# Optimization experiments

Measured on AMD Instinct MI355X. Metric: run time of the kernel, lower is better.

The kernel has to match this reference:

```python
import jax, jax.numpy as jnp
import numpy as np

NEMB = 512
NEMBDIM = 64
NHIDDEN = 1024
NINPUT = 784
COMMIT_COST = 0.25


def setup_inputs() -> dict:
    key = jax.random.key(0)
    ks = jax.random.split(key, 16)
    B = 32768
    x = jax.random.uniform(ks[0], (B, NINPUT), dtype=jnp.float32)
    # codebook: uniform(-1/nemb, 1/nemb) as in torch init
    emb = jax.random.uniform(ks[1], (NEMB, NEMBDIM), dtype=jnp.float32,
                             minval=-1.0 / NEMB, maxval=1.0 / NEMB)
    s = 0.02
    We1 = jax.random.normal(ks[2], (NHIDDEN, NINPUT), dtype=jnp.float32) * s
    be1 = jnp.zeros((NHIDDEN,), jnp.float32)
    We2 = jax.random.normal(ks[3], (NHIDDEN, NHIDDEN), dtype=jnp.float32) * s
    be2 = jnp.zeros((NHIDDEN,), jnp.float32)
    We3 = jax.random.normal(ks[4], (NEMBDIM, NHIDDEN), dtype=jnp.float32) * s
    be3 = jnp.zeros((NEMBDIM,), jnp.float32)
    Wd1 = jax.random.normal(ks[5], (NHIDDEN, NEMBDIM), dtype=jnp.float32) * s
    bd1 = jnp.zeros((NHIDDEN,), jnp.float32)
    Wd2 = jax.random.normal(ks[6], (NHIDDEN, NHIDDEN), dtype=jnp.float32) * s
    bd2 = jnp.zeros((NHIDDEN,), jnp.float32)
    Wd3 = jax.random.normal(ks[7], (NINPUT, NHIDDEN), dtype=jnp.float32) * s
    bd3 = jnp.zeros((NINPUT,), jnp.float32)
    return dict(x=x, emb=emb, We1=We1, be1=be1, We2=We2, be2=be2, We3=We3, be3=be3,
                Wd1=Wd1, bd1=bd1, Wd2=Wd2, bd2=bd2, Wd3=Wd3, bd3=bd3)


def reference(x, emb, We1, be1, We2, be2, We3, be3, Wd1, bd1, Wd2, bd2, Wd3, bd3):
    # Encoder MLP (dropout inactive at inference)
    h = jax.nn.relu(x @ We1.T + be1)
    h = jax.nn.relu(h @ We2.T + be2)
    z = h @ We3.T + be3  # [B, nembdim]

    # VQ codebook lookup. NOTE: original code omits the factor 2 on the cross
    # term (sum(z^2) + sum(e^2) - z @ e.T); we reproduce it faithfully.
    d = (jnp.sum(z * z, axis=1, keepdims=True)
         + jnp.sum(emb * emb, axis=1)
         - z @ emb.T)  # [B, nemb]
    idx = jnp.argmin(d, axis=1)  # [B]
    q = emb[idx]  # gather == one-hot @ emb, same math

    code_loss = jnp.mean((q - jax.lax.stop_gradient(z)) ** 2)
    commit_loss = jnp.mean((jax.lax.stop_gradient(q) - z) ** 2)
    loss = code_loss + COMMIT_COST * commit_loss

    # straight-through estimator
    q_st = z + jax.lax.stop_gradient(q - z)

    # Decoder MLP
    h = jax.nn.relu(q_st @ Wd1.T + bd1)
    h = jax.nn.relu(h @ Wd2.T + bd2)
    out = jax.nn.sigmoid(h @ Wd3.T + bd3)
    return out, loss
```

## Files before the change

### kernel.cpp

```cpp
#include <hip/hip_runtime.h>
#include <stdint.h>
#include <stddef.h>

typedef __bf16 bf16x8 __attribute__((ext_vector_type(8)));
typedef float  f32x4  __attribute__((ext_vector_type(4)));
typedef float  f32x16 __attribute__((ext_vector_type(16)));
typedef int    i32x8  __attribute__((ext_vector_type(8)));
typedef unsigned short u16;
typedef unsigned char  u8;

#define NIN   784
#define NINP  832
#define NH    1024
#define NE    512
#define ND    64
#define NOUTP 1024

#define BAR()   asm volatile("s_barrier" ::: "memory")
#define LGKM0() asm volatile("s_waitcnt lgkmcnt(0)" ::: "memory")
#define VM4()   asm volatile("s_waitcnt vmcnt(4)" ::: "memory")
#define VM3()   asm volatile("s_waitcnt vmcnt(3)" ::: "memory")
#define VM0()   asm volatile("s_waitcnt vmcnt(0)" ::: "memory")
#define FSWZ(r) (((r) ^ ((r) >> 2)) & 3)
#define SCL1    0x7F7F7F7F
#define GLDS(g, l) __builtin_amdgcn_global_load_lds((__attribute__((address_space(1))) void*)(g), (__attribute__((address_space(3))) void*)(l), 16, 0, 0)

struct int4x2 { int4 a, b; };

static __device__ __forceinline__ u16 f2bf(float f) {
  union { float f; unsigned u; } v; v.f = f;
  unsigned r = v.u + 0x7fffu + ((v.u >> 16) & 1u);
  return (u16)(r >> 16);
}
static __device__ __forceinline__ float bf2f(u16 b) {
  union { unsigned u; float f; } v; v.u = ((unsigned)b) << 16; return v.f;
}
static __device__ __forceinline__ unsigned pack4fp8(float a, float b, float c, float d) {
  unsigned p;
  asm("v_cvt_pk_fp8_f32 %0, %1, %2" : "=v"(p) : "v"(a), "v"(b));
  asm("v_cvt_pk_fp8_f32 %0, %1, %2 op_sel:[0,0,1]" : "+v"(p) : "v"(c), "v"(d));
  return p;
}
static __device__ __forceinline__ u8 f2fp8(float a) {
  unsigned p;
  asm("v_cvt_pk_fp8_f32 %0, %1, %2" : "=v"(p) : "v"(a), "v"(a));
  return (u8)(p & 0xff);
}

static __device__ __forceinline__ size_t t8off(int r, int c, int Cp) {
  return ((size_t)(r >> 8) * (Cp >> 6) + (c >> 6)) * 16384
       + ((r & 255) << 6) + ((((c >> 4) & 3) ^ FSWZ(r)) << 4) + (c & 15);
}

__global__ void cast_tiled8(const float* __restrict__ src, u8* __restrict__ dst,
                            int R, int C, int Cp) {
  int r = blockIdx.y;
  int c4 = (blockIdx.x * blockDim.x + threadIdx.x) * 4;
  if (c4 >= Cp) return;
  unsigned o = 0;
  if (r < R && c4 < C) {
    const float4 v = *(const float4*)&src[(size_t)r * C + c4];
    o = pack4fp8(v.x, v.y, v.z, v.w);
  }
  *(unsigned*)&dst[t8off(r, c4, Cp)] = o;
}

__global__ void prep_weights(const float* __restrict__ We1, const float* __restrict__ We2,
                             const float* __restrict__ Wd1, const float* __restrict__ Wd2,
                             const float* __restrict__ Wd3, const float* __restrict__ We3,
                             u8* __restrict__ d0, u8* __restrict__ d1, u8* __restrict__ d2,
                             u8* __restrict__ d3, u8* __restrict__ d4, u8* __restrict__ d5) {
  int id = blockIdx.z, r = blockIdx.y;
  int c4 = threadIdx.x * 4;
  const float* src; u8* dst; int R, C, Cp; bool rm = false;
  switch (id) {
    case 0: src = We1; dst = d0; R = 1024; C = NIN;  Cp = NINP; break;
    case 1: src = We2; dst = d1; R = 1024; C = 1024; Cp = 1024; break;
    case 2: src = Wd1; dst = d2; R = 1024; C = 64;   Cp = 64;   break;
    case 3: src = Wd2; dst = d3; R = 1024; C = 1024; Cp = 1024; break;
    case 4: src = Wd3; dst = d4; R = NIN;  C = 1024; Cp = 1024; break;
    default: src = We3; dst = d5; R = 64;  C = 1024; Cp = 1024; rm = true; break;
  }
  if (c4 >= Cp || (rm && r >= R)) return;
  unsigned o = 0;
  if (r < R && c4 < C) {
    const float4 v = *(const float4*)&src[(size_t)r * C + c4];
    o = pack4fp8(v.x, v.y, v.z, v.w);
  }
  if (rm) *(unsigned*)&dst[(size_t)r * Cp + c4] = o;
  else    *(unsigned*)&dst[t8off(r, c4, Cp)] = o;
}

__global__ void emb_prep(const float* __restrict__ emb, u16* __restrict__ ebf,
                         float* __restrict__ cvec, float* __restrict__ lossa,
                         unsigned* __restrict__ tick) {
  int j = blockIdx.x, l = threadIdx.x;
  if (j == 0 && l == 0) { lossa[0] = 0.f; tick[0] = 0u; }
  float v = emb[j * ND + l];
  ebf[j * 64 + (((l >> 3) ^ (j & 7)) << 3) + (l & 7)] = f2bf(v);
  float s = v * v;
  #pragma unroll
  for (int off = 32; off > 0; off >>= 1) s += __shfl_down(s, off);
  if (l == 0) cvec[j] = s;
}

template <int ACT, int OMODE, bool NCHK>
__global__ __launch_bounds__(256, 3)
void gemm128mx(const u8* __restrict__ A, const u8* __restrict__ Bm,
               const float* __restrict__ bias, float* __restrict__ Cf,
               u8* __restrict__ Cb, int N, int K, int ldc, int ntiles) {
  __shared__ __attribute__((aligned(128))) u8 lds[32768];
  const int tid = threadIdx.x, lane = tid & 63, w = tid >> 6;
  const int wr = w >> 1, wc = w & 1;
  const int l31 = lane & 31, h = lane >> 5;

  int nwg = gridDim.x, cpx = nwg >> 3, b = blockIdx.x;
  int sb = (b & 7) * cpx + (b >> 3);
  int tm = sb / ntiles, tn = sb % ntiles;

  const int NT = K >> 6;
  const u8* Ap = A + (size_t)(tm >> 1) * NT * 16384 + (size_t)(tm & 1) * 8192;
  const u8* Bp = Bm + (size_t)(tn >> 1) * NT * 16384 + (size_t)(tn & 1) * 8192;

  auto stage = [&](int t, int buf) {
    #pragma unroll
    for (int i = 0; i < 2; ++i)
      GLDS(Ap + (size_t)t * 16384 + ((i * 256 + tid) << 4),
           lds + buf * 8192 + ((i * 256 + w * 64) << 4));
    #pragma unroll
    for (int i = 0; i < 2; ++i)
      GLDS(Bp + (size_t)t * 16384 + ((i * 256 + tid) << 4),
           lds + 16384 + buf * 8192 + ((i * 256 + w * 64) << 4));
  };

  f32x16 acc[2][2] = {};
  stage(0, 0);
  if (NT > 1) stage(1, 1);

  for (int t = 0; t < NT; ++t) {
    const int buf = t & 1;
    if (t + 1 < NT) { VM4(); } else { VM0(); }
    BAR();
    const u8* lA = lds + buf * 8192;
    const u8* lB = lds + 16384 + buf * 8192;
    i32x8 af[2], bf_[2];
    #pragma unroll
    for (int s = 0; s < 2; ++s) {
      int row = wr * 64 + s * 32 + l31;
      int F = FSWZ(row);
      const u8* base = lA + row * 64;
      int4 lo = *(const int4*)&base[(((h << 1)    ) ^ F) << 4];
      int4 hi = *(const int4*)&base[(((h << 1) | 1) ^ F) << 4];
      af[s] = __builtin_bit_cast(i32x8, (int4x2){lo, hi});
    }
    #pragma unroll
    for (int s = 0; s < 2; ++s) {
      int row = wc * 64 + s * 32 + l31;
      int F = FSWZ(row);
      const u8* base = lB + row * 64;
      int4 lo = *(const int4*)&base[(((h << 1)    ) ^ F) << 4];
      int4 hi = *(const int4*)&base[(((h << 1) | 1) ^ F) << 4];
      bf_[s] = __builtin_bit_cast(i32x8, (int4x2){lo, hi});
    }
    LGKM0();
    BAR();
    if (t + 2 < NT) stage(t + 2, buf);
    #pragma unroll
    for (int ms = 0; ms < 2; ++ms)
      #pragma unroll
      for (int ns = 0; ns < 2; ++ns)
        acc[ms][ns] = __builtin_amdgcn_mfma_scale_f32_32x32x64_f8f6f4(
            af[ms], bf_[ns], acc[ms][ns], 0, 0, 0, SCL1, 0, SCL1);
  }

  float bv[2];
  #pragma unroll
  for (int ns = 0; ns < 2; ++ns) {
    int col = tn * 128 + wc * 64 + ns * 32 + l31;
    bv[ns] = (!NCHK || col < N) ? bias[col] : 0.f;
  }

  if (OMODE == 0) {
    #pragma unroll
    for (int ms = 0; ms < 2; ++ms)
      #pragma unroll
      for (int r = 0; r < 16; ++r) {
        int row = tm * 128 + wr * 64 + ms * 32 + (r & 3) + ((r >> 2) << 3) + (h << 2);
        #pragma unroll
        for (int ns = 0; ns < 2; ++ns) {
          int col = tn * 128 + wc * 64 + ns * 32 + l31;
          if (NCHK && col >= N) continue;
          float v = acc[ms][ns][r] + bv[ns];
          if (ACT == 1) v = fmaxf(v, 0.f);
          if (ACT == 2) v = 1.f / (1.f + __expf(-v));
          Cf[(size_t)row * ldc + col] = v;
        }
      }
  } else {
    float* lf = (float*)lds;
    #pragma unroll
    for (int p = 0; p < 2; ++p) {
      __syncthreads();
      if (wr == p) {
        #pragma unroll
        for (int ms = 0; ms < 2; ++ms)
          #pragma unroll
          for (int r = 0; r < 16; ++r) {
            int lrow = ms * 32 + (r & 3) + ((r >> 2) << 3) + (h << 2);
            #pragma unroll
            for (int ns = 0; ns < 2; ++ns) {
              int col = wc * 64 + ns * 32 + l31;
              float v = acc[ms][ns][r] + bv[ns];
              if (ACT == 1) v = fmaxf(v, 0.f);
              lf[lrow * 128 + (((col >> 2) ^ (lrow & 31)) << 2) + (col & 3)] = v;
            }
          }
      }
      __syncthreads();
      #pragma unroll
      for (int it = 0; it < 2; ++it) {
        int idx = it * 256 + tid;
        int lrow = idx >> 3, cc = idx & 7;
        f32x4 q[4];
        #pragma unroll
        for (int s = 0; s < 4; ++s)
          q[s] = *(const f32x4*)&lf[lrow * 128 + (((cc * 4 + s) ^ (lrow & 31)) << 2)];
        int R = tm * 128 + p * 64 + lrow;
        int C = tn * 128 + cc * 16;
        int4 o;
        o.x = pack4fp8(q[0][0], q[0][1], q[0][2], q[0][3]);
        o.y = pack4fp8(q[1][0], q[1][1], q[1][2], q[1][3]);
        o.z = pack4fp8(q[2][0], q[2][1], q[2][2], q[2][3]);
        o.w = pack4fp8(q[3][0], q[3][1], q[3][2], q[3][3]);
        *(int4*)&Cb[t8off(R, C, ldc)] = o;
      }
    }
  }
}

__global__ __launch_bounds__(256, 1)
void z_vq(const u8* __restrict__ Atiled, const u8* __restrict__ Wrm,
          const float* __restrict__ be3, const u16* __restrict__ ebf,
          const float* __restrict__ cvec, u8* __restrict__ qb8,
          float* __restrict__ lossacc, unsigned* __restrict__ tick,
          float* __restrict__ out_loss, float denom) {
  __shared__ u8 lsA[2][128 * 64];
  __shared__ u8 lsW[2][64 * 64];
  __shared__ u16 embl[512 * 64];
  __shared__ float zls[128 * 68];
  __shared__ int bidxl[128];

  const int t = threadIdx.x;
  const int lane = t & 63;
  const int w = t >> 6;
  const int lr = lane & 15, hi = lane >> 4;
  const int tm = blockIdx.x;

  #pragma unroll
  for (int i = 0; i < 16; ++i) {
    const u16* g = ebf + (size_t)((i * 256 + t) << 3);
    u16* l = embl + (size_t)((i * 256 + w * 64) << 3);
    GLDS(g, l);
  }

  const size_t abase0 = ((size_t)(tm >> 1) * 16) * 16384 + (size_t)(tm & 1) * 8192;
  auto stageA = [&](int kt, int buf) {
    #pragma unroll
    for (int i = 0; i < 2; ++i) {
      const u8* g = Atiled + abase0 + (size_t)kt * 16384 + ((i * 256 + t) << 4);
      u8* l = lsA[buf] + ((i * 256 + w * 64) << 4);
      GLDS(g, l);
    }
  };
  auto stageW = [&](int kt, int buf) {
    int row = w * 16 + (lane >> 2), p = lane & 3;
    const u8* g = Wrm + (size_t)row * 1024 + kt * 64 + ((p ^ FSWZ(row)) << 4);
    u8* l = lsW[buf] + ((w * 64) << 4);
    GLDS(g, l);
  };

  f32x4 acc[2][4] = {};
  stageA(0, 0); stageW(0, 0);
  stageA(1, 1); stageW(1, 1);
  for (int kt = 0; kt < 16; ++kt) {
    const int bf = kt & 1;
    if (kt < 15) { VM3(); } else { VM0(); }
    BAR();
    #pragma unroll
    for (int kk = 0; kk < 64; kk += 32) {
      long af[2], bfr[4];
      #pragma unroll
      for (int m = 0; m < 2; ++m) {
        int row = w * 32 + m * 16 + lr;
        int ch = ((kk >> 4) + (hi >> 1)) ^ FSWZ(row);
        af[m] = *(const long*)&lsA[bf][row * 64 + ch * 16 + ((hi & 1) << 3)];
      }
      #pragma unroll
      for (int n = 0; n < 4; ++n) {
        int row = n * 16 + lr;
        int ch = ((kk >> 4) + (hi >> 1)) ^ FSWZ(row);
        bfr[n] = *(const long*)&lsW[bf][row * 64 + ch * 16 + ((hi & 1) << 3)];
      }
      #pragma unroll
      for (int m = 0; m < 2; ++m)
        #pragma unroll
        for (int n = 0; n < 4; ++n)
          acc[m][n] = __builtin_amdgcn_mfma_f32_16x16x32_fp8_fp8(af[m], bfr[n], acc[m][n], 0, 0, 0);
    }
    LGKM0();
    BAR();
    if (kt + 2 < 16) { stageA(kt + 2, bf); stageW(kt + 2, bf); }
  }

  #pragma unroll
  for (int m = 0; m < 2; ++m)
    #pragma unroll
    for (int j = 0; j < 4; ++j) {
      int row = w * 32 + m * 16 + hi * 4 + j;
      #pragma unroll
      for (int n = 0; n < 4; ++n) {
        int col = n * 16 + lr;
        zls[row * 68 + col] = acc[m][n][j] + be3[col];
      }
    }
  __syncthreads();

  bf16x8 azf[2][2];
  #pragma unroll
  for (int rt = 0; rt < 2; ++rt)
    #pragma unroll
    for (int kf = 0; kf < 2; ++kf) {
      int row = w * 32 + rt * 16 + lr;
      union { bf16x8 v; u16 u[8]; } pk;
      #pragma unroll
      for (int e = 0; e < 8; ++e)
        pk.u[e] = f2bf(zls[row * 68 + kf * 32 + hi * 8 + e]);
      azf[rt][kf] = pk.v;
    }

  float bvv[2][4]; int bii[2][4];
  #pragma unroll
  for (int rt = 0; rt < 2; ++rt)
    #pragma unroll
    for (int j = 0; j < 4; ++j) { bvv[rt][j] = 3.4e38f; bii[rt][j] = 0; }

  for (int ct = 0; ct < 32; ++ct) {
    bf16x8 bqf[2];
    #pragma unroll
    for (int kf = 0; kf < 2; ++kf) {
      int row = ct * 16 + lr;
      int ch = (kf * 4 + hi) ^ (row & 7);
      bqf[kf] = *(const bf16x8*)&embl[row * 64 + ch * 8];
    }
    float cv = cvec[ct * 16 + lr];
    #pragma unroll
    for (int rt = 0; rt < 2; ++rt) {
      f32x4 sc = {};
      sc = __builtin_amdgcn_mfma_f32_16x16x32_bf16(azf[rt][0], bqf[0], sc, 0, 0, 0);
      sc = __builtin_amdgcn_mfma_f32_16x16x32_bf16(azf[rt][1], bqf[1], sc, 0, 0, 0);
      int code = ct * 16 + lr;
      #pragma unroll
      for (int j = 0; j < 4; ++j) {
        float d = cv - sc[j];
        if (d < bvv[rt][j]) { bvv[rt][j] = d; bii[rt][j] = code; }
      }
    }
  }
  #pragma unroll
  for (int off = 1; off < 16; off <<= 1) {
    #pragma unroll
    for (int rt = 0; rt < 2; ++rt)
      #pragma unroll
      for (int j = 0; j < 4; ++j) {
        float ov = __shfl_xor(bvv[rt][j], off);
        int   oi = __shfl_xor(bii[rt][j], off);
        if (ov < bvv[rt][j] || (ov == bvv[rt][j] && oi < bii[rt][j])) {
          bvv[rt][j] = ov; bii[rt][j] = oi;
        }
      }
  }
  if (lr == 0) {
    #pragma unroll
    for (int rt = 0; rt < 2; ++rt)
      #pragma unroll
      for (int j = 0; j < 4; ++j)
        bidxl[w * 32 + rt * 16 + hi * 4 + j] = bii[rt][j];
  }
  __syncthreads();

  const int gr0 = tm * 128;
  float ls = 0.f;
  #pragma unroll 4
  for (int r8 = 0; r8 < 32; ++r8) {
    int row = w * 32 + r8;
    int bi = bidxl[row];
    u16 qu = embl[bi * 64 + (((lane >> 3) ^ (bi & 7)) << 3) + (lane & 7)];
    float qf = bf2f(qu);
    float d = qf - zls[row * 68 + lane];
    ls += d * d;
    int R = gr0 + row;
    qb8[(size_t)R * 64 + ((((lane >> 4) & 3) ^ FSWZ(R)) << 4) + (lane & 15)] = f2fp8(qf);
  }
  #pragma unroll
  for (int off = 32; off > 0; off >>= 1) ls += __shfl_down(ls, off);
  if (lane == 0) atomicAdd(lossacc, ls);

  __syncthreads();
  if (t == 0) {
    __threadfence();
    unsigned tk = atomicAdd(tick, 1u);
    if (tk == gridDim.x - 1) {
      float v = atomicAdd(lossacc, 0.f);
      out_loss[0] = v * 1.25f / denom;
    }
  }
}

extern "C" void kernel_launch(void* const* d_in, const int* in_sizes, int n_in,
                              void* d_out, int out_size, void* d_ws, size_t ws_size,
                              hipStream_t stream) {
  const float* x   = (const float*)d_in[0];
  const float* emb = (const float*)d_in[1];
  const float* We1 = (const float*)d_in[2];
  const float* be1 = (const float*)d_in[3];
  const float* We2 = (const float*)d_in[4];
  const float* be2 = (const float*)d_in[5];
  const float* We3 = (const float*)d_in[6];
  const float* be3 = (const float*)d_in[7];
  const float* Wd1 = (const float*)d_in[8];
  const float* bd1 = (const float*)d_in[9];
  const float* Wd2 = (const float*)d_in[10];
  const float* bd2 = (const float*)d_in[11];
  const float* Wd3 = (const float*)d_in[12];
  const float* bd3 = (const float*)d_in[13];

  const int Bn = in_sizes[0] / NIN;
  float* out = (float*)d_out;
  float* out_loss = out + (size_t)Bn * NIN;

  char* ws = (char*)d_ws;
  size_t off = 0;
  auto take = [&](size_t bytes) { char* p = ws + off; off += (bytes + 255) & ~(size_t)255; return p; };

  u8*    xpad8 = (u8*)take((size_t)Bn * NINP);
  u8*    hA8   = (u8*)take((size_t)Bn * NH);
  u8*    hB8   = (u8*)take((size_t)Bn * NH);
  u8*    qb8   = (u8*)take((size_t)Bn * ND);
  u8*    we1p8 = (u8*)take((size_t)NH * NINP);
  u8*    we2b8 = (u8*)take((size_t)NH * NH);
  u8*    we3r8 = (u8*)take((size_t)64 * NH);
  u8*    wd1b8 = (u8*)take((size_t)NH * ND);
  u8*    wd2b8 = (u8*)take((size_t)NH * NH);
  u8*    wd3p8 = (u8*)take((size_t)NOUTP * NH);
  u16*   embb  = (u16*)take((size_t)NE * ND * 2);
  float* cvec  = (float*)take(NE * 4);
  float* lossa = (float*)take(4);
  unsigned* tick = (unsigned*)take(4);

  cast_tiled8<<<dim3(1, Bn), 256, 0, stream>>>(x, xpad8, Bn, NIN, NINP);
  prep_weights<<<dim3(1, 1024, 6), 256, 0, stream>>>(We1, We2, Wd1, Wd2, Wd3, We3,
                                                     we1p8, we2b8, wd1b8, wd2b8, wd3p8, we3r8);
  emb_prep<<<NE, 64, 0, stream>>>(emb, embb, cvec, lossa, tick);

  const int mt = Bn / 128;
  gemm128mx<1,1,false><<<mt * 8, 256, 0, stream>>>(xpad8, we1p8, be1, nullptr, hA8, NH, NINP, NH, 8);
  gemm128mx<1,1,false><<<mt * 8, 256, 0, stream>>>(hA8, we2b8, be2, nullptr, hB8, NH, NH, NH, 8);
  z_vq<<<Bn / 128, 256, 0, stream>>>(hB8, we3r8, be3, embb, cvec, qb8, lossa, tick,
                                     out_loss, (float)Bn * ND);
  gemm128mx<1,1,false><<<mt * 8, 256, 0, stream>>>(qb8, wd1b8, bd1, nullptr, hA8, NH, 64, NH, 8);
  gemm128mx<1,1,false><<<mt * 8, 256, 0, stream>>>(hA8, wd2b8, bd2, nullptr, hB8, NH, NH, NH, 8);
  gemm128mx<2,0,true ><<<mt * 7, 256, 0, stream>>>(hB8, wd3p8, bd3, out, nullptr, NIN, NH, NIN, 7);
}
```

Baseline: 255.9 us.

## Load GEMM B operand directly to registers, halve LDS, and retile input cast

The GEMM kernel stops staging the weight (B) tile through LDS and instead prefetches it from global memory straight into registers one K-step ahead. LDS drops from 32KB to 16KB and launch bounds rise to 4 waves per SIMD to raise occupancy. The epilogue is split into four 32-row passes so it fits the smaller LDS. The input cast kernel is also retiled so each thread writes a full 16-byte swizzled chunk. The trade-offs are higher register pressure and B reads from global or cache without the LDS reuse, since each wave column reloads its B rows.

```diff
diff --git a/kernel.cpp b/kernel.cpp
--- a/kernel.cpp
+++ b/kernel.cpp
@@ -18,8 +18,8 @@
 
 #define BAR()   asm volatile("s_barrier" ::: "memory")
 #define LGKM0() asm volatile("s_waitcnt lgkmcnt(0)" ::: "memory")
-#define VM4()   asm volatile("s_waitcnt vmcnt(4)" ::: "memory")
 #define VM3()   asm volatile("s_waitcnt vmcnt(3)" ::: "memory")
+#define VM2()   asm volatile("s_waitcnt vmcnt(2)" ::: "memory")
 #define VM0()   asm volatile("s_waitcnt vmcnt(0)" ::: "memory")
 #define FSWZ(r) (((r) ^ ((r) >> 2)) & 3)
 #define SCL1    0x7F7F7F7F
@@ -54,15 +54,33 @@
 
 __global__ void cast_tiled8(const float* __restrict__ src, u8* __restrict__ dst,
                             int R, int C, int Cp) {
-  int r = blockIdx.y;
-  int c4 = (blockIdx.x * blockDim.x + threadIdx.x) * 4;
-  if (c4 >= Cp) return;
-  unsigned o = 0;
-  if (r < R && c4 < C) {
-    const float4 v = *(const float4*)&src[(size_t)r * C + c4];
-    o = pack4fp8(v.x, v.y, v.z, v.w);
-  }
-  *(unsigned*)&dst[t8off(r, c4, Cp)] = o;
+  int kt = blockIdx.x;
+  int r = blockIdx.y * 64 + (threadIdx.x >> 2);
+  int c16 = (threadIdx.x & 3) << 4;
+  int c = kt * 64 + c16;
+  float4 v[4] = {};
+  if (r < R) {
+    #pragma unroll
+    for (int j = 0; j < 4; ++j) {
+      int cc = c + j * 4;
+      if (cc + 3 < C) {
+        v[j] = *(const float4*)&src[(size_t)r * C + cc];
+      } else {
+        float tmp[4] = {0.f, 0.f, 0.f, 0.f};
+        #pragma unroll
+        for (int e = 0; e < 4; ++e) if (cc + e < C) tmp[e] = src[(size_t)r * C + cc + e];
+        v[j] = make_float4(tmp[0], tmp[1], tmp[2], tmp[3]);
+      }
+    }
+  }
+  int4 o;
+  o.x = pack4fp8(v[0].x, v[0].y, v[0].z, v[0].w);
+  o.y = pack4fp8(v[1].x, v[1].y, v[1].z, v[1].w);
+  o.z = pack4fp8(v[2].x, v[2].y, v[2].z, v[2].w);
+  o.w = pack4fp8(v[3].x, v[3].y, v[3].z, v[3].w);
+  size_t off = ((size_t)(r >> 8) * (Cp >> 6) + kt) * 16384
+             + ((r & 255) << 6) + ((((c16 >> 4) ^ FSWZ(r)) & 3) << 4);
+  *(int4*)&dst[off] = o;
 }
 
 __global__ void prep_weights(const float* __restrict__ We1, const float* __restrict__ We2,
@@ -105,11 +123,11 @@
 }
 
 template <int ACT, int OMODE, bool NCHK>
-__global__ __launch_bounds__(256, 3)
+__global__ __launch_bounds__(256, 4)
 void gemm128mx(const u8* __restrict__ A, const u8* __restrict__ Bm,
                const float* __restrict__ bias, float* __restrict__ Cf,
                u8* __restrict__ Cb, int N, int K, int ldc, int ntiles) {
-  __shared__ __attribute__((aligned(128))) u8 lds[32768];
+  __shared__ __attribute__((aligned(128))) u8 lds[16384];
   const int tid = threadIdx.x, lane = tid & 63, w = tid >> 6;
   const int wr = w >> 1, wc = w & 1;
   const int l31 = lane & 31, h = lane >> 5;
@@ -122,28 +140,40 @@
   const u8* Ap = A + (size_t)(tm >> 1) * NT * 16384 + (size_t)(tm & 1) * 8192;
   const u8* Bp = Bm + (size_t)(tn >> 1) * NT * 16384 + (size_t)(tn & 1) * 8192;
 
-  auto stage = [&](int t, int buf) {
+  auto stageA = [&](int t, int buf) {
     #pragma unroll
     for (int i = 0; i < 2; ++i)
       GLDS(Ap + (size_t)t * 16384 + ((i * 256 + tid) << 4),
            lds + buf * 8192 + ((i * 256 + w * 64) << 4));
-    #pragma unroll
-    for (int i = 0; i < 2; ++i)
-      GLDS(Bp + (size_t)t * 16384 + ((i * 256 + tid) << 4),
-           lds + 16384 + buf * 8192 + ((i * 256 + w * 64) << 4));
   };
 
+  int brow[2], bF[2];
+  #pragma unroll
+  for (int s = 0; s < 2; ++s) { brow[s] = wc * 64 + s * 32 + l31; bF[s] = FSWZ(brow[s]); }
+  auto loadB = [&](int t, i32x8* dstv) {
+    #pragma unroll
+    for (int s = 0; s < 2; ++s) {
+      const u8* base = Bp + (size_t)t * 16384 + brow[s] * 64;
+      int4 lo = *(const int4*)&base[(((h << 1)    ) ^ bF[s]) << 4];
+      int4 hi = *(const int4*)&base[(((h << 1) | 1) ^ bF[s]) << 4];
+      dstv[s] = __builtin_bit_cast(i32x8, (int4x2){lo, hi});
+    }
+  };
+
   f32x16 acc[2][2] = {};
-  stage(0, 0);
-  if (NT > 1) stage(1, 1);
+  i32x8 bcur[2], bnxt[2];
+
+  stageA(0, 0);
+  loadB(0, bcur);
+  if (NT > 1) stageA(1, 1);
 
   for (int t = 0; t < NT; ++t) {
     const int buf = t & 1;
-    if (t + 1 < NT) { VM4(); } else { VM0(); }
+    if (t + 1 < NT) { VM2(); } else { VM0(); }
     BAR();
+    if (t > 0) { bcur[0] = bnxt[0]; bcur[1] = bnxt[1]; }
     const u8* lA = lds + buf * 8192;
-    const u8* lB = lds + 16384 + buf * 8192;
-    i32x8 af[2], bf_[2];
+    i32x8 af[2];
     #pragma unroll
     for (int s = 0; s < 2; ++s) {
       int row = wr * 64 + s * 32 + l31;
@@ -153,24 +183,16 @@
       int4 hi = *(const int4*)&base[(((h << 1) | 1) ^ F) << 4];
       af[s] = __builtin_bit_cast(i32x8, (int4x2){lo, hi});
     }
-    #pragma unroll
-    for (int s = 0; s < 2; ++s) {
-      int row = wc * 64 + s * 32 + l31;
-      int F = FSWZ(row);
-      const u8* base = lB + row * 64;
-      int4 lo = *(const int4*)&base[(((h << 1)    ) ^ F) << 4];
-      int4 hi = *(const int4*)&base[(((h << 1) | 1) ^ F) << 4];
-      bf_[s] = __builtin_bit_cast(i32x8, (int4x2){lo, hi});
-    }
+    if (t + 1 < NT) loadB(t + 1, bnxt);
     LGKM0();
     BAR();
-    if (t + 2 < NT) stage(t + 2, buf);
+    if (t + 2 < NT) stageA(t + 2, buf);
     #pragma unroll
     for (int ms = 0; ms < 2; ++ms)
       #pragma unroll
       for (int ns = 0; ns < 2; ++ns)
         acc[ms][ns] = __builtin_amdgcn_mfma_scale_f32_32x32x64_f8f6f4(
-            af[ms], bf_[ns], acc[ms][ns], 0, 0, 0, SCL1, 0, SCL1);
+            af[ms], bcur[ns], acc[ms][ns], 0, 0, 0, SCL1, 0, SCL1);
   }
 
   float bv[2];
@@ -199,33 +221,30 @@
   } else {
     float* lf = (float*)lds;
     #pragma unroll
-    for (int p = 0; p < 2; ++p) {
+    for (int p = 0; p < 4; ++p) {
       __syncthreads();
-      if (wr == p) {
+      if (wr == (p >> 1)) {
+        const int ms = p & 1;
         #pragma unroll
-        for (int ms = 0; ms < 2; ++ms)
+        for (int r = 0; r < 16; ++r) {
+          int lrow = (r & 3) + ((r >> 2) << 3) + (h << 2);
           #pragma unroll
-          for (int r = 0; r < 16; ++r) {
-            int lrow = ms * 32 + (r & 3) + ((r >> 2) << 3) + (h << 2);
-            #pragma unroll
-            for (int ns = 0; ns < 2; ++ns) {
-              int col = wc * 64 + ns * 32 + l31;
-              float v = acc[ms][ns][r] + bv[ns];
-              if (ACT == 1) v = fmaxf(v, 0.f);
-              lf[lrow * 128 + (((col >> 2) ^ (lrow & 31)) << 2) + (col & 3)] = v;
-            }
+          for (int ns = 0; ns < 2; ++ns) {
+            int col = wc * 64 + ns * 32 + l31;
+            float v = acc[ms][ns][r] + bv[ns];
+            if (ACT == 1) v = fmaxf(v, 0.f);
+            lf[lrow * 128 + (((col >> 2) ^ lrow) << 2) + (col & 3)] = v;
           }
+        }
       }
       __syncthreads();
-      #pragma unroll
-      for (int it = 0; it < 2; ++it) {
-        int idx = it * 256 + tid;
-        int lrow = idx >> 3, cc = idx & 7;
+      {
+        int lrow = tid >> 3, cc = tid & 7;
         f32x4 q[4];
         #pragma unroll
         for (int s = 0; s < 4; ++s)
-          q[s] = *(const f32x4*)&lf[lrow * 128 + (((cc * 4 + s) ^ (lrow & 31)) << 2)];
-        int R = tm * 128 + p * 64 + lrow;
+          q[s] = *(const f32x4*)&lf[lrow * 128 + (((cc * 4 + s) ^ lrow) << 2)];
+        int R = tm * 128 + p * 32 + lrow;
         int C = tn * 128 + cc * 16;
         int4 o;
         o.x = pack4fp8(q[0][0], q[0][1], q[0][2], q[0][3]);
@@ -457,7 +476,7 @@
   float* lossa = (float*)take(4);
   unsigned* tick = (unsigned*)take(4);
 
-  cast_tiled8<<<dim3(1, Bn), 256, 0, stream>>>(x, xpad8, Bn, NIN, NINP);
+  cast_tiled8<<<dim3(NINP / 64, Bn / 64), 256, 0, stream>>>(x, xpad8, Bn, NIN, NINP);
   prep_weights<<<dim3(1, 1024, 6), 256, 0, stream>>>(We1, We2, Wd1, Wd2, Wd3, We3,
                                                      we1p8, we2b8, wd1b8, wd2b8, wd3p8, we3r8);
   emb_prep<<<NE, 64, 0, stream>>>(emb, embb, cvec, lossa, tick);
```

After: 282.5 us. +10.4%, slower.
